# Kernel optimization log

Measured on AMD Instinct MI355X. Metric: run time of the kernel, lower is better.

Reference implementation:

```python
import jax, jax.numpy as jnp
import numpy as np

N = 100000
E = 1600000
IN_DIM = 256
HID = 64


def setup_inputs() -> dict:
    key = jax.random.key(0)
    k1, k2, k3 = jax.random.split(key, 3)
    x = jax.random.normal(k1, (N, IN_DIM), dtype=jnp.float32)
    edge_index = jax.random.randint(k2, (2, E), 0, N, dtype=jnp.int64)
    # glorot-ish init for GCNConv weight, zero bias (PyG default)
    W = jax.random.normal(k3, (IN_DIM, HID), dtype=jnp.float32) * (1.0 / np.sqrt(IN_DIM))
    b = jnp.zeros((HID,), dtype=jnp.float32)
    return {"x": x, "edge_index": edge_index, "W": W, "b": b}


def reference(x, edge_index, W, b):
    # GCNConv: out = D^{-1/2} (A + I) D^{-1/2} (X W) + b
    n = x.shape[0]
    # add self-loops
    loop = jnp.arange(n, dtype=edge_index.dtype)
    src = jnp.concatenate([edge_index[0], loop])  # [E+N]
    dst = jnp.concatenate([edge_index[1], loop])  # [E+N]
    # degree of target nodes (incl. self-loops)
    deg = jax.ops.segment_sum(jnp.ones_like(dst, dtype=x.dtype), dst, num_segments=n)
    dinv = jnp.where(deg > 0, jax.lax.rsqrt(deg), 0.0)  # deg^{-1/2}, inf->0
    norm = dinv[src] * dinv[dst]  # [E+N]
    h = x @ W  # [N, HID] transform before aggregation
    msg = h[src] * norm[:, None]  # gather + scale, [E+N, HID]
    out = jax.ops.segment_sum(msg, dst, num_segments=n)  # scatter-add
    return out + b
```

## Files before the change

kernel.cpp:

```cpp
#include <hip/hip_runtime.h>

typedef float floatx4 __attribute__((ext_vector_type(4)));
typedef short s16x8 __attribute__((ext_vector_type(8)));

#define WG 256
#define NBUCK 512
#define BSH 8
#define EBLK 512
#define CAP 8192

__device__ inline unsigned pack_bf16_rne(float a, float b) {
    unsigned ua = __float_as_uint(a), ub = __float_as_uint(b);
    ua = (ua + 0x7FFFu + ((ua >> 16) & 1u)) >> 16;
    ub = (ub + 0x7FFFu + ((ub >> 16) & 1u)) >> 16;
    return ua | (ub << 16);
}

union FragU {
    unsigned u[4];
    uint4 q;
    s16x8 v;
};

__global__ __launch_bounds__(WG) void k_build(const void* __restrict__ ei, int* __restrict__ cursor,
                                              unsigned* __restrict__ ebuf, int E) {
    __shared__ int h[NBUCK];
    __shared__ int base[NBUCK];
    __shared__ int s32flag;
    const int t = threadIdx.x;
    if (t == 0) s32flag = 0;
    for (int i = t; i < NBUCK; i += WG) h[i] = 0;
    __syncthreads();
    {
        const int* w = (const int*)ei;
        int nz = 0;
        for (int j = t; j < 4096; j += WG) nz |= (w[2 * j + 1] != 0);
        if (nz) atomicOr(&s32flag, 1);
    }
    __syncthreads();
    const bool i32 = (s32flag != 0);
    const int chunk = (E + EBLK - 1) / EBLK;
    const int s = blockIdx.x * chunk;
    const int eend = min(E, s + chunk);
    if (i32) {
        const int* pd = (const int*)ei + E;
        for (int e = s + t; e < eend; e += WG) atomicAdd(&h[pd[e] >> BSH], 1);
    } else {
        const long long* pd = (const long long*)ei + E;
        for (int e = s + t; e < eend; e += WG) atomicAdd(&h[(int)pd[e] >> BSH], 1);
    }
    __syncthreads();
    for (int i = t; i < NBUCK; i += WG) {
        int c = h[i];
        base[i] = c ? atomicAdd(&cursor[i], c) : 0;
        h[i] = 0;
    }
    __syncthreads();
    for (int e = s + t; e < eend; e += WG) {
        int sN, dN;
        if (i32) {
            const int* p = (const int*)ei;
            sN = p[e];
            dN = p[E + e];
        } else {
            const long long* p = (const long long*)ei;
            sN = (int)p[e];
            dN = (int)p[(long long)E + e];
        }
        int bkt = dN >> BSH;
        int pos = base[bkt] + atomicAdd(&h[bkt], 1);
        if (pos < CAP) ebuf[(size_t)bkt * CAP + pos] = (unsigned)sN | ((unsigned)(dN & 255) << 24);
    }
}

__global__ __launch_bounds__(WG) void k_csr(const unsigned* __restrict__ ebuf, const int* __restrict__ cursor,
                                            int* __restrict__ off, int* __restrict__ srcs,
                                            float* __restrict__ dinv, int N, int nbuse) {
    __shared__ int red[WG];
    __shared__ int h[256];
    __shared__ int sc[256];
    __shared__ int cur[256];
    const int t = threadIdx.x;
    const int b = blockIdx.x;
    const int node0 = b << BSH;
    const int rows = min(256, N - node0);
    int part = 0;
    for (int i = t; i < b; i += WG) part += min(cursor[i], CAP);
    red[t] = part;
    h[t] = 0;
    __syncthreads();
    for (int d = WG / 2; d > 0; d >>= 1) {
        if (t < d) red[t] += red[t + d];
        __syncthreads();
    }
    const int ebase = red[0];
    const int cnt = min(cursor[b], CAP);
    const unsigned* eb = ebuf + (size_t)b * CAP;
    for (int j = t; j < cnt; j += WG) atomicAdd(&h[eb[j] >> 24], 1);
    __syncthreads();
    const int deg = (t < rows) ? h[t] + 1 : 0;
    sc[t] = deg;
    __syncthreads();
    for (int d = 1; d < 256; d <<= 1) {
        int a = (t >= d) ? sc[t - d] : 0;
        __syncthreads();
        sc[t] += a;
        __syncthreads();
    }
    const int basef = ebase + node0;
    const int local = sc[t] - deg;
    if (t < rows) {
        off[node0 + t] = basef + local;
        srcs[basef + local] = node0 + t;
        cur[t] = local + 1;
        dinv[node0 + t] = rsqrtf((float)deg);
    }
    if (b == nbuse - 1 && t == 0) off[N] = ebase + cnt + N;
    __syncthreads();
    for (int j = t; j < cnt; j += WG) {
        unsigned w = eb[j];
        int dl = (int)(w >> 24);
        int pos = basef + atomicAdd(&cur[dl], 1);
        srcs[pos] = (int)(w & 0xFFFFFFu);
    }
}

__global__ __launch_bounds__(WG) void k_gemm(const float* __restrict__ x, const float* __restrict__ W,
                                             const float* __restrict__ dinv, unsigned short* __restrict__ g,
                                             int N) {
    __shared__ unsigned Wf[2048 * 4];

    const int t = threadIdx.x;
    for (int q = t; q < 2048; q += WG) {
        const int kb = q >> 8, nt = (q >> 6) & 3, ln = q & 63;
        const int quad = ln >> 4, l15 = ln & 15;
        const int col = nt * 16 + l15;
        const int krow = kb * 32 + quad * 8;
        unsigned up[4];
#pragma unroll
        for (int p = 0; p < 4; p++) {
            float a = W[(krow + 2 * p) * 64 + col];
            float b = W[(krow + 2 * p + 1) * 64 + col];
            up[p] = pack_bf16_rne(a, b);
        }
        uint4 pk = {up[0], up[1], up[2], up[3]};
        *(uint4*)(&Wf[q * 4]) = pk;
    }
    __syncthreads();

    const int wv = t >> 6;
    const int lane = t & 63;
    const int quad = lane >> 4, l15 = lane & 15;

    long long arow = (long long)blockIdx.x * 64 + wv * 16 + l15;
    if (arow >= N) arow = N - 1;
    const float* xr = x + arow * 256 + quad * 8;

    floatx4 xv[8][2];
#pragma unroll
    for (int kb = 0; kb < 8; kb++) {
        xv[kb][0] = *(const floatx4*)(xr + kb * 32);
        xv[kb][1] = *(const floatx4*)(xr + kb * 32 + 4);
    }

    floatx4 acc[4];
#pragma unroll
    for (int nt = 0; nt < 4; nt++) acc[nt] = 0.f;

#pragma unroll
    for (int kb = 0; kb < 8; kb++) {
        FragU a;
        a.u[0] = pack_bf16_rne(xv[kb][0][0], xv[kb][0][1]);
        a.u[1] = pack_bf16_rne(xv[kb][0][2], xv[kb][0][3]);
        a.u[2] = pack_bf16_rne(xv[kb][1][0], xv[kb][1][1]);
        a.u[3] = pack_bf16_rne(xv[kb][1][2], xv[kb][1][3]);
#pragma unroll
        for (int nt = 0; nt < 4; nt++) {
            FragU b;
            b.q = *(const uint4*)(&Wf[((kb * 4 + nt) * 64 + lane) * 4]);
            acc[nt] = __builtin_amdgcn_mfma_f32_16x16x32_bf16(a.v, b.v, acc[nt], 0, 0, 0);
        }
    }

    const long long orow0 = (long long)blockIdx.x * 64 + wv * 16 + quad * 4;
#pragma unroll
    for (int r = 0; r < 4; r++) {
        const long long orow = orow0 + r;
        if (orow < N) {
            const float s = dinv[orow];
#pragma unroll
            for (int nt = 0; nt < 4; nt++) {
                float v = acc[nt][r] * s;
                unsigned uv = __float_as_uint(v);
                uv = (uv + 0x7FFFu + ((uv >> 16) & 1u)) >> 16;
                g[orow * 64 + nt * 16 + l15] = (unsigned short)uv;
            }
        }
    }
}

__global__ __launch_bounds__(WG) void k_gather(const unsigned short* __restrict__ g,
                                               const int* __restrict__ off, const int* __restrict__ srcs,
                                               const float* __restrict__ dinv, const float* __restrict__ bias,
                                               float* __restrict__ out, int N) {
    int wid = (blockIdx.x * WG + threadIdx.x) >> 6;
    int lane = threadIdx.x & 63;
    if (wid >= N) return;
    int grp = lane >> 3;
    int c8 = (lane & 7) * 8;
    int e0 = off[wid], e1 = off[wid + 1];
    float a0 = 0.f, a1 = 0.f, a2 = 0.f, a3 = 0.f, a4 = 0.f, a5 = 0.f, a6 = 0.f, a7 = 0.f;
    for (int e = e0 + grp; e < e1; e += 8) {
        int s = srcs[e];
        uint4 v = *(const uint4*)(g + (long long)s * 64 + c8);
        a0 += __uint_as_float(v.x << 16);
        a1 += __uint_as_float(v.x & 0xFFFF0000u);
        a2 += __uint_as_float(v.y << 16);
        a3 += __uint_as_float(v.y & 0xFFFF0000u);
        a4 += __uint_as_float(v.z << 16);
        a5 += __uint_as_float(v.z & 0xFFFF0000u);
        a6 += __uint_as_float(v.w << 16);
        a7 += __uint_as_float(v.w & 0xFFFF0000u);
    }
#pragma unroll
    for (int m = 8; m <= 32; m <<= 1) {
        a0 += __shfl_xor(a0, m, 64);
        a1 += __shfl_xor(a1, m, 64);
        a2 += __shfl_xor(a2, m, 64);
        a3 += __shfl_xor(a3, m, 64);
        a4 += __shfl_xor(a4, m, 64);
        a5 += __shfl_xor(a5, m, 64);
        a6 += __shfl_xor(a6, m, 64);
        a7 += __shfl_xor(a7, m, 64);
    }
    if (grp == 0) {
        float d = dinv[wid];
        const floatx4 b0 = *(const floatx4*)(bias + c8);
        const floatx4 b1 = *(const floatx4*)(bias + c8 + 4);
        floatx4 o0, o1;
        o0[0] = d * a0 + b0[0];
        o0[1] = d * a1 + b0[1];
        o0[2] = d * a2 + b0[2];
        o0[3] = d * a3 + b0[3];
        o1[0] = d * a4 + b1[0];
        o1[1] = d * a5 + b1[1];
        o1[2] = d * a6 + b1[2];
        o1[3] = d * a7 + b1[3];
        *(floatx4*)(out + (long long)wid * 64 + c8) = o0;
        *(floatx4*)(out + (long long)wid * 64 + c8 + 4) = o1;
    }
}

extern "C" void kernel_launch(void* const* d_in, const int* in_sizes, int n_in,
                              void* d_out, int out_size, void* d_ws, size_t ws_size,
                              hipStream_t stream) {
    const float* x = (const float*)d_in[0];
    const void* ei = d_in[1];
    const float* W = (const float*)d_in[2];
    const float* b = (const float*)d_in[3];
    float* out = (float*)d_out;

    const int N = in_sizes[0] / 256;
    const int E = in_sizes[1] / 2;
    const int NBUSE = (N + 255) >> BSH;

    char* ws = (char*)d_ws;
    size_t o = 0;
    auto alloc = [&](size_t bytes) -> void* {
        void* p = ws + o;
        o += (bytes + 255) & ~(size_t)255;
        return p;
    };
    float* dinv = (float*)alloc((size_t)N * 4);
    unsigned short* g = (unsigned short*)alloc((size_t)N * 64 * 2);
    unsigned* ebuf = (unsigned*)alloc((size_t)NBUSE * CAP * 4);
    int* cursor = (int*)alloc((size_t)NBUCK * 4);
    int* off = (int*)alloc((size_t)(N + 1) * 4);
    int* srcs = (int*)alloc((size_t)(E + N) * 4);
    if (o > ws_size) return;

    hipMemsetAsync(cursor, 0, (size_t)NBUCK * 4, stream);
    k_build<<<EBLK, WG, 0, stream>>>(ei, cursor, ebuf, E);
    k_csr<<<NBUSE, WG, 0, stream>>>(ebuf, cursor, off, srcs, dinv, N, NBUSE);
    k_gemm<<<(N + 63) / 64, WG, 0, stream>>>(x, W, dinv, g, N);
    k_gather<<<(N * 64 + WG - 1) / WG, WG, 0, stream>>>(g, off, srcs, dinv, b, out, N);
}
```

Measured before the change: 281.8 us.

## Merge CSR build and GEMM into one launch by moving source dinv scaling to gather

The CSR-building kernel and the GEMM kernel become one horizontally fused launch, with the block index deciding which role each block plays. This lets the two independent stages run concurrently and removes a launch boundary. To break the GEMM's dependency on dinv, the per-source dinv scaling moves into the gather loop, which now loads dinv[s] per edge. The gather loop also prefetches the next source index. The cost is an extra scattered 4-byte load and a multiply per edge in the gather stage.

```diff
diff --git a/kernel.cpp b/kernel.cpp
--- a/kernel.cpp
+++ b/kernel.cpp
@@ -73,127 +73,126 @@
     }
 }
 
-__global__ __launch_bounds__(WG) void k_csr(const unsigned* __restrict__ ebuf, const int* __restrict__ cursor,
+__global__ __launch_bounds__(WG) void k_mid(const unsigned* __restrict__ ebuf, const int* __restrict__ cursor,
                                             int* __restrict__ off, int* __restrict__ srcs,
-                                            float* __restrict__ dinv, int N, int nbuse) {
-    __shared__ int red[WG];
-    __shared__ int h[256];
-    __shared__ int sc[256];
-    __shared__ int cur[256];
+                                            float* __restrict__ dinv,
+                                            const float* __restrict__ x, const float* __restrict__ W,
+                                            unsigned short* __restrict__ g, int N, int nbuse) {
+    __shared__ unsigned smem[2048 * 4];
     const int t = threadIdx.x;
-    const int b = blockIdx.x;
-    const int node0 = b << BSH;
-    const int rows = min(256, N - node0);
-    int part = 0;
-    for (int i = t; i < b; i += WG) part += min(cursor[i], CAP);
-    red[t] = part;
-    h[t] = 0;
-    __syncthreads();
-    for (int d = WG / 2; d > 0; d >>= 1) {
-        if (t < d) red[t] += red[t + d];
-        __syncthreads();
-    }
-    const int ebase = red[0];
-    const int cnt = min(cursor[b], CAP);
-    const unsigned* eb = ebuf + (size_t)b * CAP;
-    for (int j = t; j < cnt; j += WG) atomicAdd(&h[eb[j] >> 24], 1);
-    __syncthreads();
-    const int deg = (t < rows) ? h[t] + 1 : 0;
-    sc[t] = deg;
-    __syncthreads();
-    for (int d = 1; d < 256; d <<= 1) {
-        int a = (t >= d) ? sc[t - d] : 0;
-        __syncthreads();
-        sc[t] += a;
-        __syncthreads();
-    }
-    const int basef = ebase + node0;
-    const int local = sc[t] - deg;
-    if (t < rows) {
-        off[node0 + t] = basef + local;
-        srcs[basef + local] = node0 + t;
-        cur[t] = local + 1;
-        dinv[node0 + t] = rsqrtf((float)deg);
-    }
-    if (b == nbuse - 1 && t == 0) off[N] = ebase + cnt + N;
-    __syncthreads();
-    for (int j = t; j < cnt; j += WG) {
-        unsigned w = eb[j];
-        int dl = (int)(w >> 24);
-        int pos = basef + atomicAdd(&cur[dl], 1);
-        srcs[pos] = (int)(w & 0xFFFFFFu);
-    }
-}
-
-__global__ __launch_bounds__(WG) void k_gemm(const float* __restrict__ x, const float* __restrict__ W,
-                                             const float* __restrict__ dinv, unsigned short* __restrict__ g,
-                                             int N) {
-    __shared__ unsigned Wf[2048 * 4];
-
-    const int t = threadIdx.x;
-    for (int q = t; q < 2048; q += WG) {
-        const int kb = q >> 8, nt = (q >> 6) & 3, ln = q & 63;
-        const int quad = ln >> 4, l15 = ln & 15;
-        const int col = nt * 16 + l15;
-        const int krow = kb * 32 + quad * 8;
-        unsigned up[4];
-#pragma unroll
-        for (int p = 0; p < 4; p++) {
-            float a = W[(krow + 2 * p) * 64 + col];
-            float b = W[(krow + 2 * p + 1) * 64 + col];
-            up[p] = pack_bf16_rne(a, b);
-        }
-        uint4 pk = {up[0], up[1], up[2], up[3]};
-        *(uint4*)(&Wf[q * 4]) = pk;
-    }
-    __syncthreads();
-
-    const int wv = t >> 6;
-    const int lane = t & 63;
-    const int quad = lane >> 4, l15 = lane & 15;
-
-    long long arow = (long long)blockIdx.x * 64 + wv * 16 + l15;
-    if (arow >= N) arow = N - 1;
-    const float* xr = x + arow * 256 + quad * 8;
-
-    floatx4 xv[8][2];
-#pragma unroll
-    for (int kb = 0; kb < 8; kb++) {
-        xv[kb][0] = *(const floatx4*)(xr + kb * 32);
-        xv[kb][1] = *(const floatx4*)(xr + kb * 32 + 4);
-    }
-
-    floatx4 acc[4];
-#pragma unroll
-    for (int nt = 0; nt < 4; nt++) acc[nt] = 0.f;
-
-#pragma unroll
-    for (int kb = 0; kb < 8; kb++) {
-        FragU a;
-        a.u[0] = pack_bf16_rne(xv[kb][0][0], xv[kb][0][1]);
-        a.u[1] = pack_bf16_rne(xv[kb][0][2], xv[kb][0][3]);
-        a.u[2] = pack_bf16_rne(xv[kb][1][0], xv[kb][1][1]);
-        a.u[3] = pack_bf16_rne(xv[kb][1][2], xv[kb][1][3]);
-#pragma unroll
-        for (int nt = 0; nt < 4; nt++) {
-            FragU b;
-            b.q = *(const uint4*)(&Wf[((kb * 4 + nt) * 64 + lane) * 4]);
-            acc[nt] = __builtin_amdgcn_mfma_f32_16x16x32_bf16(a.v, b.v, acc[nt], 0, 0, 0);
-        }
-    }
-
-    const long long orow0 = (long long)blockIdx.x * 64 + wv * 16 + quad * 4;
-#pragma unroll
-    for (int r = 0; r < 4; r++) {
-        const long long orow = orow0 + r;
-        if (orow < N) {
-            const float s = dinv[orow];
+
+    if ((int)blockIdx.x < nbuse) {
+        int* red = (int*)smem;
+        int* h = red + 256;
+        int* sc = h + 256;
+        int* cur = sc + 256;
+        const int b = blockIdx.x;
+        const int node0 = b << BSH;
+        const int rows = min(256, N - node0);
+        int part = 0;
+        for (int i = t; i < b; i += WG) part += min(cursor[i], CAP);
+        red[t] = part;
+        h[t] = 0;
+        __syncthreads();
+        for (int d = WG / 2; d > 0; d >>= 1) {
+            if (t < d) red[t] += red[t + d];
+            __syncthreads();
+        }
+        const int ebase = red[0];
+        const int cnt = min(cursor[b], CAP);
+        const unsigned* eb = ebuf + (size_t)b * CAP;
+        for (int j = t; j < cnt; j += WG) atomicAdd(&h[eb[j] >> 24], 1);
+        __syncthreads();
+        const int deg = (t < rows) ? h[t] + 1 : 0;
+        sc[t] = deg;
+        __syncthreads();
+        for (int d = 1; d < 256; d <<= 1) {
+            int a = (t >= d) ? sc[t - d] : 0;
+            __syncthreads();
+            sc[t] += a;
+            __syncthreads();
+        }
+        const int basef = ebase + node0;
+        const int local = sc[t] - deg;
+        if (t < rows) {
+            off[node0 + t] = basef + local;
+            srcs[basef + local] = node0 + t;
+            cur[t] = local + 1;
+            dinv[node0 + t] = rsqrtf((float)deg);
+        }
+        if (b == nbuse - 1 && t == 0) off[N] = ebase + cnt + N;
+        __syncthreads();
+        for (int j = t; j < cnt; j += WG) {
+            unsigned w = eb[j];
+            int dl = (int)(w >> 24);
+            int pos = basef + atomicAdd(&cur[dl], 1);
+            srcs[pos] = (int)(w & 0xFFFFFFu);
+        }
+    } else {
+        const int bb = blockIdx.x - nbuse;
+        for (int q = t; q < 2048; q += WG) {
+            const int kb = q >> 8, nt = (q >> 6) & 3, ln = q & 63;
+            const int quad = ln >> 4, l15 = ln & 15;
+            const int col = nt * 16 + l15;
+            const int krow = kb * 32 + quad * 8;
+            unsigned up[4];
+#pragma unroll
+            for (int p = 0; p < 4; p++) {
+                float a = W[(krow + 2 * p) * 64 + col];
+                float b2 = W[(krow + 2 * p + 1) * 64 + col];
+                up[p] = pack_bf16_rne(a, b2);
+            }
+            uint4 pk = {up[0], up[1], up[2], up[3]};
+            *(uint4*)(&smem[q * 4]) = pk;
+        }
+        __syncthreads();
+
+        const int wv = t >> 6;
+        const int lane = t & 63;
+        const int quad = lane >> 4, l15 = lane & 15;
+
+        long long arow = (long long)bb * 64 + wv * 16 + l15;
+        if (arow >= N) arow = N - 1;
+        const float* xr = x + arow * 256 + quad * 8;
+
+        floatx4 xv[8][2];
+#pragma unroll
+        for (int kb = 0; kb < 8; kb++) {
+            xv[kb][0] = *(const floatx4*)(xr + kb * 32);
+            xv[kb][1] = *(const floatx4*)(xr + kb * 32 + 4);
+        }
+
+        floatx4 acc[4];
+#pragma unroll
+        for (int nt = 0; nt < 4; nt++) acc[nt] = 0.f;
+
+#pragma unroll
+        for (int kb = 0; kb < 8; kb++) {
+            FragU a;
+            a.u[0] = pack_bf16_rne(xv[kb][0][0], xv[kb][0][1]);
+            a.u[1] = pack_bf16_rne(xv[kb][0][2], xv[kb][0][3]);
+            a.u[2] = pack_bf16_rne(xv[kb][1][0], xv[kb][1][1]);
+            a.u[3] = pack_bf16_rne(xv[kb][1][2], xv[kb][1][3]);
 #pragma unroll
             for (int nt = 0; nt < 4; nt++) {
-                float v = acc[nt][r] * s;
-                unsigned uv = __float_as_uint(v);
-                uv = (uv + 0x7FFFu + ((uv >> 16) & 1u)) >> 16;
-                g[orow * 64 + nt * 16 + l15] = (unsigned short)uv;
+                FragU b2;
+                b2.q = *(const uint4*)(&smem[((kb * 4 + nt) * 64 + lane) * 4]);
+                acc[nt] = __builtin_amdgcn_mfma_f32_16x16x32_bf16(a.v, b2.v, acc[nt], 0, 0, 0);
+            }
+        }
+
+        const long long orow0 = (long long)bb * 64 + wv * 16 + quad * 4;
+#pragma unroll
+        for (int r = 0; r < 4; r++) {
+            const long long orow = orow0 + r;
+            if (orow < N) {
+#pragma unroll
+                for (int nt = 0; nt < 4; nt++) {
+                    float v = acc[nt][r];
+                    unsigned uv = __float_as_uint(v);
+                    uv = (uv + 0x7FFFu + ((uv >> 16) & 1u)) >> 16;
+                    g[orow * 64 + nt * 16 + l15] = (unsigned short)uv;
+                }
             }
         }
     }
@@ -210,17 +209,23 @@
     int c8 = (lane & 7) * 8;
     int e0 = off[wid], e1 = off[wid + 1];
     float a0 = 0.f, a1 = 0.f, a2 = 0.f, a3 = 0.f, a4 = 0.f, a5 = 0.f, a6 = 0.f, a7 = 0.f;
-    for (int e = e0 + grp; e < e1; e += 8) {
-        int s = srcs[e];
+    int e = e0 + grp;
+    int s = (e < e1) ? srcs[e] : 0;
+    while (e < e1) {
+        int en = e + 8;
+        int sn = (en < e1) ? srcs[en] : 0;
+        float ds = dinv[s];
         uint4 v = *(const uint4*)(g + (long long)s * 64 + c8);
-        a0 += __uint_as_float(v.x << 16);
-        a1 += __uint_as_float(v.x & 0xFFFF0000u);
-        a2 += __uint_as_float(v.y << 16);
-        a3 += __uint_as_float(v.y & 0xFFFF0000u);
-        a4 += __uint_as_float(v.z << 16);
-        a5 += __uint_as_float(v.z & 0xFFFF0000u);
-        a6 += __uint_as_float(v.w << 16);
-        a7 += __uint_as_float(v.w & 0xFFFF0000u);
+        a0 += ds * __uint_as_float(v.x << 16);
+        a1 += ds * __uint_as_float(v.x & 0xFFFF0000u);
+        a2 += ds * __uint_as_float(v.y << 16);
+        a3 += ds * __uint_as_float(v.y & 0xFFFF0000u);
+        a4 += ds * __uint_as_float(v.z << 16);
+        a5 += ds * __uint_as_float(v.z & 0xFFFF0000u);
+        a6 += ds * __uint_as_float(v.w << 16);
+        a7 += ds * __uint_as_float(v.w & 0xFFFF0000u);
+        s = sn;
+        e = en;
     }
 #pragma unroll
     for (int m = 8; m <= 32; m <<= 1) {
@@ -263,6 +268,7 @@
     const int N = in_sizes[0] / 256;
     const int E = in_sizes[1] / 2;
     const int NBUSE = (N + 255) >> BSH;
+    const int GEMMB = (N + 63) / 64;
 
     char* ws = (char*)d_ws;
     size_t o = 0;
@@ -281,7 +287,6 @@
 
     hipMemsetAsync(cursor, 0, (size_t)NBUCK * 4, stream);
     k_build<<<EBLK, WG, 0, stream>>>(ei, cursor, ebuf, E);
-    k_csr<<<NBUSE, WG, 0, stream>>>(ebuf, cursor, off, srcs, dinv, N, NBUSE);
-    k_gemm<<<(N + 63) / 64, WG, 0, stream>>>(x, W, dinv, g, N);
+    k_mid<<<NBUSE + GEMMB, WG, 0, stream>>>(ebuf, cursor, off, srcs, dinv, x, W, g, N, NBUSE);
     k_gather<<<(N * 64 + WG - 1) / WG, WG, 0, stream>>>(g, off, srcs, dinv, b, out, N);
 }
```

After: 269.3 us. 4.5% less time.
